# Kernel tuning notes

Measured on AMD Instinct MI355X. Metric: run time of the kernel, lower is better.

The kernel has to match this reference:

```python
import jax, jax.numpy as jnp
import numpy as np

N_NODES = 50000
N_EDGES = 800000
D = 128
L = 3


def setup_inputs() -> dict:
    key = jax.random.key(0)
    k1, k2, k3 = jax.random.split(key, 3)
    x = jax.random.normal(k1, (N_NODES, D), dtype=jnp.float32)
    edge_index = jax.random.randint(k2, (2, N_EDGES), 0, N_NODES, dtype=jnp.int64)
    # per-layer GCNConv weights [L, in, out], bias [L, out] (zeros, as nn.Linear default bias is small),
    # PReLU per-channel slopes initialized to 0.25 (torch default)
    Ws = jax.random.normal(k3, (L, D, D), dtype=jnp.float32) / np.sqrt(D)
    bs = jnp.zeros((L, D), dtype=jnp.float32)
    alphas = jnp.full((L, D), 0.25, dtype=jnp.float32)
    return {"x": x, "edge_index": edge_index, "Ws": Ws, "bs": bs, "alphas": alphas}


def reference(x, edge_index, Ws, bs, alphas):
    N = x.shape[0]
    # PyG gcn_norm with edge_weight=None: unit weights, add self-loops (fill value 1),
    # symmetric normalization deg^{-1/2}[row] * deg^{-1/2}[col], aggregate at col (target).
    loop = jnp.arange(N, dtype=edge_index.dtype)
    row = jnp.concatenate([edge_index[0], loop])  # [E+N] source
    col = jnp.concatenate([edge_index[1], loop])  # [E+N] target
    deg = jax.ops.segment_sum(jnp.ones(row.shape[0], x.dtype), col, num_segments=N)
    dinv = jax.lax.rsqrt(deg)  # deg >= 1 due to self-loops
    norm = dinv[row] * dinv[col]  # [E+N]

    z = x
    for l in range(Ws.shape[0]):
        h = z @ Ws[l]  # linear transform [N, D]
        # gather -> scale -> scatter-add aggregation
        agg = jax.ops.segment_sum(h[row] * norm[:, None], col, num_segments=N)
        out = agg + bs[l]
        z = jnp.where(out >= 0, out, alphas[l] * out)  # per-channel PReLU
    return z
```

## Files before the change

kernel.cpp:

```cpp
#include <hip/hip_runtime.h>

#define N_NODES 50000
#define N_EDGES 800000
#define D 128
#define L 3
#define CAP 56

typedef __attribute__((ext_vector_type(8))) short short8;
typedef __attribute__((ext_vector_type(16))) float f32x16;

__device__ __forceinline__ unsigned int bf16_rne(float f) {
  unsigned int u = __float_as_uint(f);
  return (u + 0x7FFFu + ((u >> 16) & 1u)) >> 16;
}


__global__ __launch_bounds__(256) void zero_k(unsigned int* deg) {
  int i = blockIdx.x * 256 + threadIdx.x;
  if (i < N_NODES) deg[i] = 0u;
}

__global__ __launch_bounds__(256) void build_k(const int* __restrict__ rows,
                                               const int* __restrict__ cols,
                                               unsigned int* deg,
                                               unsigned int* __restrict__ csr) {
  int e = blockIdx.x * 256 + threadIdx.x;
  if (e >= N_EDGES) return;
  int c = cols[e];
  unsigned int r = atomicAdd(&deg[c], 1u);
  if (r < CAP) csr[(size_t)c * CAP + r] = (unsigned int)rows[e];
}

__global__ __launch_bounds__(256) void dinv_k(float* dinv_f, const unsigned int* deg) {
  int i = blockIdx.x * 256 + threadIdx.x;
  if (i < N_NODES) dinv_f[i] = rsqrtf((float)(deg[i] + 1u));
}

__global__ __launch_bounds__(256) void gather_k(const unsigned int* __restrict__ deg,
                                                const unsigned int* __restrict__ csr,
                                                const float* __restrict__ dinv,
                                                const float* __restrict__ Z,
                                                float* __restrict__ AGG) {
  int wid = (blockIdx.x * 256 + threadIdx.x) >> 6;
  int lane = threadIdx.x & 63;
  if (wid >= N_NODES) return;
  const float2* Z2 = (const float2*)Z;
  float di = dinv[wid];
  float2 z = Z2[(size_t)wid * 64 + lane];
  float sx = di * z.x, sy = di * z.y;
  unsigned int cnt = deg[wid];
  if (cnt > CAP) cnt = CAP;
  unsigned int s = 0u;
  float w = 0.f;
  if (lane < (int)cnt) {
    s = csr[(size_t)wid * CAP + lane];
    w = dinv[s];
  }
  unsigned int j = 0;
  for (; j + 8u <= cnt; j += 8u) {
    unsigned int ss[8];
    float wws[8];
#pragma unroll
    for (int t = 0; t < 8; ++t) {
      ss[t] = __shfl(s, (int)(j + t), 64);
      wws[t] = __shfl(w, (int)(j + t), 64);
    }
    float2 v[8];
#pragma unroll
    for (int t = 0; t < 8; ++t) v[t] = Z2[(size_t)ss[t] * 64 + lane];
#pragma unroll
    for (int t = 0; t < 8; ++t) {
      sx += wws[t] * v[t].x;
      sy += wws[t] * v[t].y;
    }
  }
  for (; j < cnt; ++j) {
    unsigned int s0 = __shfl(s, (int)j, 64);
    float w0 = __shfl(w, (int)j, 64);
    float2 v0 = Z2[(size_t)s0 * 64 + lane];
    sx += w0 * v0.x;
    sy += w0 * v0.y;
  }
  float2 r;
  r.x = sx * di;
  r.y = sy * di;
  ((float2*)AGG)[(size_t)wid * 64 + lane] = r;
}

__global__ __launch_bounds__(256) void gemm_mfma_k(const float* __restrict__ P,
                                                   const float* __restrict__ W,
                                                   const float* __restrict__ bias,
                                                   const float* __restrict__ alpha,
                                                   float* __restrict__ out) {
  __shared__ unsigned int sWhi[128 * 36];
  __shared__ unsigned int sWlo[128 * 36];
  const int tid = threadIdx.x;
  const int lane = tid & 63;
  const int w = tid >> 6;
  const int kg = lane >> 5;
  const int cl = lane & 31;
  const int rb = blockIdx.x * 128;
  const int row = rb + w * 32 + cl;
  const int ar = row < N_NODES ? row : N_NODES - 1;

  f32x16 acc[4];
#pragma unroll
  for (int cf = 0; cf < 4; ++cf)
#pragma unroll
    for (int j = 0; j < 16; ++j) acc[cf][j] = 0.f;

  for (int h = 0; h < 2; ++h) {
    const int k0 = h * 64;
    if (h) __syncthreads();
#pragma unroll
    for (int j = 0; j < 16; ++j) {
      int id = j * 256 + tid;
      int c = id & 127;
      int kd = id >> 7;
      float w0 = W[(size_t)(k0 + kd * 2) * 128 + c];
      float w1 = W[(size_t)(k0 + kd * 2 + 1) * 128 + c];
      unsigned int h0 = bf16_rne(w0), h1 = bf16_rne(w1);
      float f0 = __uint_as_float(h0 << 16), f1 = __uint_as_float(h1 << 16);
      unsigned int l0 = bf16_rne(w0 - f0), l1 = bf16_rne(w1 - f1);
      sWhi[c * 36 + kd] = h0 | (h1 << 16);
      sWlo[c * 36 + kd] = l0 | (l1 << 16);
    }
    __syncthreads();

#pragma unroll
    for (int ks4 = 0; ks4 < 4; ++ks4) {
      const float4* ap = (const float4*)(P + (size_t)ar * D + k0 + ks4 * 16 + kg * 8);
      float4 a0 = ap[0], a1 = ap[1];
      float af[8] = {a0.x, a0.y, a0.z, a0.w, a1.x, a1.y, a1.z, a1.w};
      short8 ahi, alo;
#pragma unroll
      for (int i = 0; i < 8; ++i) {
        unsigned int hb = bf16_rne(af[i]);
        float hf = __uint_as_float(hb << 16);
        unsigned int lb = bf16_rne(af[i] - hf);
        ahi[i] = (short)hb;
        alo[i] = (short)lb;
      }
#pragma unroll
      for (int cf = 0; cf < 4; ++cf) {
        int cc = cf * 32 + cl;
        int off = cc * 36 + ks4 * 8 + kg * 4;
        short8 bhi = *(const short8*)&sWhi[off];
        short8 blo = *(const short8*)&sWlo[off];
        acc[cf] = __builtin_amdgcn_mfma_f32_32x32x16_bf16(ahi, bhi, acc[cf], 0, 0, 0);
        acc[cf] = __builtin_amdgcn_mfma_f32_32x32x16_bf16(ahi, blo, acc[cf], 0, 0, 0);
        acc[cf] = __builtin_amdgcn_mfma_f32_32x32x16_bf16(alo, bhi, acc[cf], 0, 0, 0);
      }
    }
  }

#pragma unroll
  for (int cf = 0; cf < 4; ++cf) {
    int col = cf * 32 + cl;
    float bl = bias[col], al = alpha[col];
#pragma unroll
    for (int j = 0; j < 16; ++j) {
      int r = rb + w * 32 + 4 * kg + (j & 3) + 8 * (j >> 2);
      if (r < N_NODES) {
        float v = acc[cf][j] + bl;
        out[(size_t)r * D + col] = v >= 0.f ? v : al * v;
      }
    }
  }
}


extern "C" void kernel_launch(void* const* d_in, const int* in_sizes, int n_in,
                              void* d_out, int out_size, void* d_ws, size_t ws_size,
                              hipStream_t stream) {
  const float* x      = (const float*)d_in[0];
  const int*   ei     = (const int*)d_in[1];
  const float* Ws     = (const float*)d_in[2];
  const float* bs     = (const float*)d_in[3];
  const float* alphas = (const float*)d_in[4];
  float* out = (float*)d_out;

  const int* rows = ei;
  const int* cols = ei + N_EDGES;

  char* ws = (char*)d_ws;
  const size_t NPAD = (((size_t)N_NODES * 4 + 255) / 256) * 256;
  const size_t CSRPAD = (((size_t)N_NODES * CAP * 4 + 255) / 256) * 256;
  float*        dinv = (float*)ws;         ws += NPAD;
  unsigned int* deg  = (unsigned int*)ws;  ws += NPAD;
  unsigned int* csr  = (unsigned int*)ws;  ws += CSRPAD;
  float*        AGG  = (float*)ws;
  float* Z = out;

  zero_k<<<(N_NODES + 255) / 256, 256, 0, stream>>>(deg);
  build_k<<<(N_EDGES + 255) / 256, 256, 0, stream>>>(rows, cols, deg, csr);
  dinv_k<<<(N_NODES + 255) / 256, 256, 0, stream>>>(dinv, deg);

  for (int l = 0; l < L; ++l) {
    const float* zin = (l == 0) ? x : Z;
    gather_k<<<(N_NODES * 64 + 255) / 256, 256, 0, stream>>>(deg, csr, dinv, zin, AGG);
    gemm_mfma_k<<<(N_NODES + 127) / 128, 256, 0, stream>>>(
        AGG, Ws + (size_t)l * D * D, bs + (size_t)l * D, alphas + (size_t)l * D, Z);
  }
}
```

Before: 297.0 us.

## Precompute bf16 hi/lo weight splits and emit split aggregates from gather

Weights for all layers are split into bf16 hi/lo pairs once, in a separate kernel, and stored in a K-packed layout in global memory. The gather kernel now writes its output as packed bf16 hi/lo words, so the GEMM no longer converts fp32 inputs. The GEMM drops its LDS staging and barriers, runs one wave per 32-row block, and reads the B fragments directly from global or L2. This removes the per-block weight conversion and the fp32 activation reads, but it moves B-operand reads from LDS to cache and launches many small blocks.

```diff
diff --git a/kernel.cpp b/kernel.cpp
--- a/kernel.cpp
+++ b/kernel.cpp
@@ -36,11 +36,30 @@
   if (i < N_NODES) dinv_f[i] = rsqrtf((float)(deg[i] + 1u));
 }
 
+__global__ __launch_bounds__(256) void wconv_k(const float* __restrict__ Ws,
+                                               unsigned int* __restrict__ Whi,
+                                               unsigned int* __restrict__ Wlo) {
+  int id = blockIdx.x * 256 + threadIdx.x;
+  if (id >= L * 128 * 64) return;
+  int kd = id & 63;
+  int c = (id >> 6) & 127;
+  int l = id >> 13;
+  const float* W = Ws + (size_t)l * D * D;
+  float w0 = W[(size_t)(2 * kd) * 128 + c];
+  float w1 = W[(size_t)(2 * kd + 1) * 128 + c];
+  unsigned int h0 = bf16_rne(w0), h1 = bf16_rne(w1);
+  float f0 = __uint_as_float(h0 << 16), f1 = __uint_as_float(h1 << 16);
+  unsigned int l0 = bf16_rne(w0 - f0), l1 = bf16_rne(w1 - f1);
+  Whi[id] = h0 | (h1 << 16);
+  Wlo[id] = l0 | (l1 << 16);
+}
+
 __global__ __launch_bounds__(256) void gather_k(const unsigned int* __restrict__ deg,
                                                 const unsigned int* __restrict__ csr,
                                                 const float* __restrict__ dinv,
                                                 const float* __restrict__ Z,
-                                                float* __restrict__ AGG) {
+                                                unsigned int* __restrict__ AGGhi,
+                                                unsigned int* __restrict__ AGGlo) {
   int wid = (blockIdx.x * 256 + threadIdx.x) >> 6;
   int lane = threadIdx.x & 63;
   if (wid >= N_NODES) return;
@@ -81,26 +100,27 @@
     sx += w0 * v0.x;
     sy += w0 * v0.y;
   }
-  float2 r;
-  r.x = sx * di;
-  r.y = sy * di;
-  ((float2*)AGG)[(size_t)wid * 64 + lane] = r;
-}
-
-__global__ __launch_bounds__(256) void gemm_mfma_k(const float* __restrict__ P,
-                                                   const float* __restrict__ W,
-                                                   const float* __restrict__ bias,
-                                                   const float* __restrict__ alpha,
-                                                   float* __restrict__ out) {
-  __shared__ unsigned int sWhi[128 * 36];
-  __shared__ unsigned int sWlo[128 * 36];
-  const int tid = threadIdx.x;
-  const int lane = tid & 63;
-  const int w = tid >> 6;
+  sx *= di;
+  sy *= di;
+  unsigned int hx = bf16_rne(sx), hy = bf16_rne(sy);
+  float fx = __uint_as_float(hx << 16), fy = __uint_as_float(hy << 16);
+  unsigned int lx = bf16_rne(sx - fx), ly = bf16_rne(sy - fy);
+  AGGhi[(size_t)wid * 64 + lane] = hx | (hy << 16);
+  AGGlo[(size_t)wid * 64 + lane] = lx | (ly << 16);
+}
+
+__global__ __launch_bounds__(64) void gemm_mfma_k(const unsigned int* __restrict__ Phi,
+                                                  const unsigned int* __restrict__ Plo,
+                                                  const unsigned int* __restrict__ Whi,
+                                                  const unsigned int* __restrict__ Wlo,
+                                                  const float* __restrict__ bias,
+                                                  const float* __restrict__ alpha,
+                                                  float* __restrict__ out) {
+  const int lane = threadIdx.x;
   const int kg = lane >> 5;
   const int cl = lane & 31;
-  const int rb = blockIdx.x * 128;
-  const int row = rb + w * 32 + cl;
+  const int rb = blockIdx.x * 32;
+  const int row = rb + cl;
   const int ar = row < N_NODES ? row : N_NODES - 1;
 
   f32x16 acc[4];
@@ -109,48 +129,19 @@
 #pragma unroll
     for (int j = 0; j < 16; ++j) acc[cf][j] = 0.f;
 
-  for (int h = 0; h < 2; ++h) {
-    const int k0 = h * 64;
-    if (h) __syncthreads();
-#pragma unroll
-    for (int j = 0; j < 16; ++j) {
-      int id = j * 256 + tid;
-      int c = id & 127;
-      int kd = id >> 7;
-      float w0 = W[(size_t)(k0 + kd * 2) * 128 + c];
-      float w1 = W[(size_t)(k0 + kd * 2 + 1) * 128 + c];
-      unsigned int h0 = bf16_rne(w0), h1 = bf16_rne(w1);
-      float f0 = __uint_as_float(h0 << 16), f1 = __uint_as_float(h1 << 16);
-      unsigned int l0 = bf16_rne(w0 - f0), l1 = bf16_rne(w1 - f1);
-      sWhi[c * 36 + kd] = h0 | (h1 << 16);
-      sWlo[c * 36 + kd] = l0 | (l1 << 16);
-    }
-    __syncthreads();
-
-#pragma unroll
-    for (int ks4 = 0; ks4 < 4; ++ks4) {
-      const float4* ap = (const float4*)(P + (size_t)ar * D + k0 + ks4 * 16 + kg * 8);
-      float4 a0 = ap[0], a1 = ap[1];
-      float af[8] = {a0.x, a0.y, a0.z, a0.w, a1.x, a1.y, a1.z, a1.w};
-      short8 ahi, alo;
-#pragma unroll
-      for (int i = 0; i < 8; ++i) {
-        unsigned int hb = bf16_rne(af[i]);
-        float hf = __uint_as_float(hb << 16);
-        unsigned int lb = bf16_rne(af[i] - hf);
-        ahi[i] = (short)hb;
-        alo[i] = (short)lb;
-      }
-#pragma unroll
-      for (int cf = 0; cf < 4; ++cf) {
-        int cc = cf * 32 + cl;
-        int off = cc * 36 + ks4 * 8 + kg * 4;
-        short8 bhi = *(const short8*)&sWhi[off];
-        short8 blo = *(const short8*)&sWlo[off];
-        acc[cf] = __builtin_amdgcn_mfma_f32_32x32x16_bf16(ahi, bhi, acc[cf], 0, 0, 0);
-        acc[cf] = __builtin_amdgcn_mfma_f32_32x32x16_bf16(ahi, blo, acc[cf], 0, 0, 0);
-        acc[cf] = __builtin_amdgcn_mfma_f32_32x32x16_bf16(alo, bhi, acc[cf], 0, 0, 0);
-      }
+#pragma unroll
+  for (int ks = 0; ks < 8; ++ks) {
+    int pb = ks * 8 + kg * 4;
+    short8 ahi = *(const short8*)&Phi[(size_t)ar * 64 + pb];
+    short8 alo = *(const short8*)&Plo[(size_t)ar * 64 + pb];
+#pragma unroll
+    for (int cf = 0; cf < 4; ++cf) {
+      int cc = cf * 32 + cl;
+      short8 bhi = *(const short8*)&Whi[(size_t)cc * 64 + pb];
+      short8 blo = *(const short8*)&Wlo[(size_t)cc * 64 + pb];
+      acc[cf] = __builtin_amdgcn_mfma_f32_32x32x16_bf16(ahi, bhi, acc[cf], 0, 0, 0);
+      acc[cf] = __builtin_amdgcn_mfma_f32_32x32x16_bf16(ahi, blo, acc[cf], 0, 0, 0);
+      acc[cf] = __builtin_amdgcn_mfma_f32_32x32x16_bf16(alo, bhi, acc[cf], 0, 0, 0);
     }
   }
 
@@ -160,7 +151,7 @@
     float bl = bias[col], al = alpha[col];
 #pragma unroll
     for (int j = 0; j < 16; ++j) {
-      int r = rb + w * 32 + 4 * kg + (j & 3) + 8 * (j >> 2);
+      int r = rb + 4 * kg + (j & 3) + 8 * (j >> 2);
       if (r < N_NODES) {
         float v = acc[cf][j] + bl;
         out[(size_t)r * D + col] = v >= 0.f ? v : al * v;
@@ -186,20 +177,27 @@
   char* ws = (char*)d_ws;
   const size_t NPAD = (((size_t)N_NODES * 4 + 255) / 256) * 256;
   const size_t CSRPAD = (((size_t)N_NODES * CAP * 4 + 255) / 256) * 256;
-  float*        dinv = (float*)ws;         ws += NPAD;
-  unsigned int* deg  = (unsigned int*)ws;  ws += NPAD;
-  unsigned int* csr  = (unsigned int*)ws;  ws += CSRPAD;
-  float*        AGG  = (float*)ws;
+  const size_t AGGPAD = (((size_t)N_NODES * 64 * 4 + 255) / 256) * 256;
+  const size_t WPAD = (((size_t)L * 128 * 64 * 4 + 255) / 256) * 256;
+  float*        dinv  = (float*)ws;         ws += NPAD;
+  unsigned int* deg   = (unsigned int*)ws;  ws += NPAD;
+  unsigned int* csr   = (unsigned int*)ws;  ws += CSRPAD;
+  unsigned int* AGGhi = (unsigned int*)ws;  ws += AGGPAD;
+  unsigned int* AGGlo = (unsigned int*)ws;  ws += AGGPAD;
+  unsigned int* Whi   = (unsigned int*)ws;  ws += WPAD;
+  unsigned int* Wlo   = (unsigned int*)ws;  ws += WPAD;
   float* Z = out;
 
   zero_k<<<(N_NODES + 255) / 256, 256, 0, stream>>>(deg);
   build_k<<<(N_EDGES + 255) / 256, 256, 0, stream>>>(rows, cols, deg, csr);
   dinv_k<<<(N_NODES + 255) / 256, 256, 0, stream>>>(dinv, deg);
+  wconv_k<<<(L * 128 * 64 + 255) / 256, 256, 0, stream>>>(Ws, Whi, Wlo);
 
   for (int l = 0; l < L; ++l) {
     const float* zin = (l == 0) ? x : Z;
-    gather_k<<<(N_NODES * 64 + 255) / 256, 256, 0, stream>>>(deg, csr, dinv, zin, AGG);
-    gemm_mfma_k<<<(N_NODES + 127) / 128, 256, 0, stream>>>(
-        AGG, Ws + (size_t)l * D * D, bs + (size_t)l * D, alphas + (size_t)l * D, Z);
-  }
-}
+    gather_k<<<(N_NODES * 64 + 255) / 256, 256, 0, stream>>>(deg, csr, dinv, zin, AGGhi, AGGlo);
+    gemm_mfma_k<<<(N_NODES + 31) / 32, 64, 0, stream>>>(
+        AGGhi, AGGlo, Whi + (size_t)l * 128 * 64, Wlo + (size_t)l * 128 * 64,
+        bs + (size_t)l * D, alphas + (size_t)l * D, Z);
+  }
+}
```

Result: slower. 318.2 us (+7.1%).
